# Performance work log

Measured on AMD Instinct MI355X. Metric: run time of the kernel, lower is better.

Reference implementation:

```python
import jax, jax.numpy as jnp
from jax import lax
import numpy as np

LOWEST_HZ = 1.0
HIGHEST_HZ = 40.0
FS = 256
ORDER = 5


def _butter_sos(order, cutoff, btype, fs):
    """Butterworth digital filter as second-order sections (scipy-equivalent math)."""
    Wn = cutoff / (0.5 * fs)
    fs2 = 2.0
    warped = 2.0 * fs2 * np.tan(np.pi * Wn / fs2)  # pre-warped analog cutoff
    m = np.arange(1, order + 1)
    p = np.exp(1j * np.pi * (2 * m + order - 1) / (2.0 * order))  # analog prototype poles
    if btype == 'lp':
        z = np.zeros(0, dtype=complex)
        p = p * warped
        k = warped ** order
    else:  # 'hp' : lp2hp transform
        k = 1.0 / np.real(np.prod(-p))
        p = warped / p
        z = np.zeros(order, dtype=complex)
    # bilinear transform (internal fs = 2)
    f2 = 2.0 * fs2
    pd = (f2 + p) / (f2 - p)
    zd = (f2 + z) / (f2 - z)
    kd = k * np.real(np.prod(f2 - z) / np.prod(f2 - p))
    zd = np.concatenate([zd, -np.ones(order - len(zd))])  # pad zeros at z=-1
    z0 = float(np.real(zd[0]))  # all digital zeros identical (z=-1 for lp, z=+1 for hp)
    real_p = [float(pp.real) for pp in pd if abs(pp.imag) < 1e-10]
    cplx_p = [pp for pp in pd if pp.imag > 1e-10]
    sos = []
    for pp in cplx_p:  # conjugate pair -> one biquad
        sos.append([1.0, -2.0 * z0, z0 * z0, 1.0, -2.0 * pp.real, float(np.real(pp * np.conj(pp)))])
    for pr in real_p:  # leftover real pole -> first-order section
        sos.append([1.0, -z0, 0.0, 1.0, -pr, 0.0])
    sos = np.array(sos, dtype=np.float64)
    sos[0, :3] *= kd  # fold overall gain into first section
    return sos


def _sosfilt(sos, x):
    """Cascaded biquad IIR (direct form II transposed), zero initial state. x: [..., T]."""
    S = sos.shape[0]
    b0, b1, b2 = sos[:, 0], sos[:, 1], sos[:, 2]
    a1, a2 = sos[:, 4], sos[:, 5]
    xT = jnp.moveaxis(x, -1, 0)  # [T, ...]
    state0 = jnp.zeros((S, 2) + xT.shape[1:], x.dtype)

    def step(state, xt):
        cur = xt
        new = []
        for i in range(S):  # fixed small cascade of 6 sections
            w1, w2 = state[i, 0], state[i, 1]
            y = b0[i] * cur + w1
            nw1 = b1[i] * cur - a1[i] * y + w2
            nw2 = b2[i] * cur - a2[i] * y
            new.append(jnp.stack([nw1, nw2]))
            cur = y
        return jnp.stack(new), cur

    _, yT = lax.scan(step, state0, xT)
    return jnp.moveaxis(yT, 0, -1)


def setup_inputs() -> dict:
    key = jax.random.key(0)
    x = jax.random.normal(key, (32, 64, 16384), dtype=jnp.float32)
    sos_hp = _butter_sos(ORDER, LOWEST_HZ, 'hp', FS)
    sos_lp = _butter_sos(ORDER, HIGHEST_HZ, 'lp', FS)
    sos = jnp.asarray(np.concatenate([sos_hp, sos_lp], axis=0), dtype=jnp.float32)  # [6,6]
    return {"x": x, "sos": sos}


def reference(x, sos):
    # highpass sections then lowpass sections = one 6-section cascade
    return _sosfilt(sos, x)
```

## Files before the change

### kernel.cpp

```cpp
#include <hip/hip_runtime.h>

#define T_LEN 16384
#define NSEC 6
#define NSTATE 12
#define NMAT (NSTATE * NSTATE)
#define NPOW 5
#define NTHR 256
#define NS_TOT 2048

__device__ float g_Mp[NPOW * NMAT];
__device__ float g_Phi[64 * NSTATE];

__device__ __forceinline__ float rfl(float v) {
    return __int_as_float(__builtin_amdgcn_readfirstlane(__float_as_int(v)));
}

__global__ void k_matpow(const float* __restrict__ sos) {
    __shared__ double A[NMAT];
    __shared__ double ph[2][NSTATE];
    int tid = threadIdx.x;

    if (tid < NSTATE) {
        double b0[NSEC], b1[NSEC], b2[NSEC], a1[NSEC], a2[NSEC];
#pragma unroll
        for (int i = 0; i < NSEC; ++i) {
            b0[i] = (double)sos[i * 6 + 0];
            b1[i] = (double)sos[i * 6 + 1];
            b2[i] = (double)sos[i * 6 + 2];
            a1[i] = (double)sos[i * 6 + 4];
            a2[i] = (double)sos[i * 6 + 5];
        }
        double w1[NSEC], w2[NSEC];
#pragma unroll
        for (int i = 0; i < NSEC; ++i) {
            w1[i] = (tid == 2 * i) ? 1.0 : 0.0;
            w2[i] = (tid == 2 * i + 1) ? 1.0 : 0.0;
        }
        double cur = 0.0;
#pragma unroll
        for (int i = 0; i < NSEC; ++i) {
            double yv = fma(b0[i], cur, w1[i]);
            double n1 = fma(b1[i], cur, fma(-a1[i], yv, w2[i]));
            double n2 = fma(b2[i], cur, -(a2[i] * yv));
            w1[i] = n1; w2[i] = n2; cur = yv;
        }
#pragma unroll
        for (int i = 0; i < NSEC; ++i) {
            A[(2 * i) * NSTATE + tid]     = w1[i];
            A[(2 * i + 1) * NSTATE + tid] = w2[i];
        }
        double c = 0.0;
        if ((tid & 1) == 0) {
            int i = tid >> 1;
            double p = 1.0;
            for (int j = i + 1; j < NSEC; ++j) p *= (double)sos[j * 6 + 0];
            c = p;
        }
        ph[0][tid] = c;
    }
    __syncthreads();

    for (int t = 0; t < 64; ++t) {
        if (tid < NSTATE) {
            g_Phi[t * NSTATE + tid] = (float)ph[t & 1][tid];
            double v = 0.0;
#pragma unroll
            for (int kk = 0; kk < NSTATE; ++kk)
                v = fma(ph[t & 1][kk], A[kk * NSTATE + tid], v);
            ph[(t + 1) & 1][tid] = v;
        }
        __syncthreads();
    }

    const int rr = tid / NSTATE, cc = tid % NSTATE;
    for (int it = 1; it <= 10; ++it) {
        double v = 0.0;
        if (tid < NMAT) {
#pragma unroll
            for (int kk = 0; kk < NSTATE; ++kk)
                v = fma(A[rr * NSTATE + kk], A[kk * NSTATE + cc], v);
        }
        __syncthreads();
        if (tid < NMAT) {
            A[rr * NSTATE + cc] = v;
            if (it >= 6) g_Mp[(it - 6) * NMAT + tid] = (float)v;
        }
        __syncthreads();
    }
}

#define TRI_MATVEC(MROW_BASE, IN, OUT, INIT_FROM)                               \
    {                                                                           \
        _Pragma("unroll")                                                       \
        for (int q = 0; q < NSTATE; ++q) {                                      \
            const int lim = 2 * (q >> 1) + 2;                                   \
            const float4* row = (const float4*)((MROW_BASE) + q * NSTATE);      \
            float acc = (INIT_FROM);                                            \
            float4 r0 = row[0];                                                 \
            acc = fmaf(r0.x, (IN)[0], acc);                                     \
            acc = fmaf(r0.y, (IN)[1], acc);                                     \
            if (lim > 2) { acc = fmaf(r0.z, (IN)[2], acc);                      \
                           acc = fmaf(r0.w, (IN)[3], acc); }                    \
            if (lim > 4) {                                                      \
                float4 r1 = row[1];                                             \
                acc = fmaf(r1.x, (IN)[4], acc);                                 \
                acc = fmaf(r1.y, (IN)[5], acc);                                 \
                if (lim > 6) { acc = fmaf(r1.z, (IN)[6], acc);                  \
                               acc = fmaf(r1.w, (IN)[7], acc); }                \
            }                                                                   \
            if (lim > 8) {                                                      \
                float4 r2 = row[2];                                             \
                acc = fmaf(r2.x, (IN)[8], acc);                                 \
                acc = fmaf(r2.y, (IN)[9], acc);                                 \
                if (lim > 10) { acc = fmaf(r2.z, (IN)[10], acc);                \
                                acc = fmaf(r2.w, (IN)[11], acc); }              \
            }                                                                   \
            (OUT)[q] = acc;                                                     \
        }                                                                       \
    }

__global__ void __launch_bounds__(NTHR, 4)
k_main(const float* __restrict__ x, const float* __restrict__ sos,
       float* __restrict__ y) {
    __shared__ float Mp[NPOW][NMAT];
    __shared__ float Ph[64 * NSTATE];
    __shared__ float cw[4][NSTATE];
    __shared__ float4 sm4[2048];

    const int k = threadIdx.x;
    const int lane = k & 63;
    const int w = k >> 6;
    const int sig = blockIdx.x;

    for (int i = k; i < NPOW * NMAT; i += NTHR)
        Mp[i / NMAT][i % NMAT] = g_Mp[i];
    for (int i = k; i < 64 * NSTATE; i += NTHR)
        Ph[i] = g_Phi[i];

    float b0[NSEC], b1[NSEC], b2[NSEC], a1[NSEC], a2[NSEC];
#pragma unroll
    for (int i = 0; i < NSEC; ++i) {
        b0[i] = rfl(sos[i * 6 + 0]);
        b1[i] = rfl(sos[i * 6 + 1]);
        b2[i] = rfl(sos[i * 6 + 2]);
        a1[i] = rfl(sos[i * 6 + 4]);
        a2[i] = rfl(sos[i * 6 + 5]);
    }

    const float4* xp4 = (const float4*)(x + (size_t)sig * T_LEN) + k * 16;
    float4 stash[16];
    float w1_[NSEC], w2_[NSEC];
#pragma unroll
    for (int i = 0; i < NSEC; ++i) { w1_[i] = 0.f; w2_[i] = 0.f; }

    auto fstep = [&](float cur) -> float {
#pragma unroll
        for (int i = 0; i < NSEC; ++i) {
            float yv = fmaf(b0[i], cur, w1_[i]);
            w1_[i] = fmaf(b1[i], cur, fmaf(-a1[i], yv, w2_[i]));
            w2_[i] = fmaf(b2[i], cur, -(a2[i] * yv));
            cur = yv;
        }
        return cur;
    };

#pragma unroll
    for (int m = 0; m < 16; ++m) {
        float4 v = xp4[m];
        v.x = fstep(v.x); v.y = fstep(v.y); v.z = fstep(v.z); v.w = fstep(v.w);
        stash[m] = v;
    }
    float c0[NSTATE];
#pragma unroll
    for (int i = 0; i < NSEC; ++i) { c0[2 * i] = w1_[i]; c0[2 * i + 1] = w2_[i]; }

    __syncthreads();

#pragma unroll
    for (int rnd = 0; rnd < NPOW; ++rnd) {
        const int d = 1 << rnd;
        float pr[NSTATE];
#pragma unroll
        for (int j = 0; j < NSTATE; ++j) pr[j] = __shfl_up(c0[j], d, 64);
        if (lane >= d) {
            float nc[NSTATE];
            TRI_MATVEC(Mp[rnd], pr, nc, c0[q]);
#pragma unroll
            for (int j = 0; j < NSTATE; ++j) c0[j] = nc[j];
        }
    }

    if (lane == 63) {
#pragma unroll
        for (int j = 0; j < NSTATE; ++j) cw[w][j] = c0[j];
    }
    __syncthreads();

    if (w > 0) {
        float v[NSTATE];
#pragma unroll
        for (int j = 0; j < NSTATE; ++j) v[j] = cw[w - 1][j];
#pragma unroll
        for (int i = 0; i < NPOW; ++i) {
            if (((lane + 1) >> i) & 1) {
                float nv[NSTATE];
                TRI_MATVEC(Mp[i], v, nv, 0.f);
#pragma unroll
                for (int j = 0; j < NSTATE; ++j) v[j] = nv[j];
            }
        }
        if (lane < 31) {
#pragma unroll
            for (int j = 0; j < NSTATE; ++j) c0[j] += v[j];
        }
    }

    float si[NSTATE];
#pragma unroll
    for (int j = 0; j < NSTATE; ++j) si[j] = __shfl_up(c0[j], 1, 64);
    if (lane == 0) {
#pragma unroll
        for (int j = 0; j < NSTATE; ++j) si[j] = (w == 0) ? 0.f : cw[w - 1][j];
    }

#pragma unroll
    for (int m = 0; m < 16; ++m) {
        float4 v = stash[m];
        float corr[4];
#pragma unroll
        for (int q = 0; q < 4; ++q) {
            const float4* ph = (const float4*)&Ph[(m * 4 + q) * NSTATE];
            float4 p0 = ph[0], p1 = ph[1], p2 = ph[2];
            float acc = p0.x * si[0];
            acc = fmaf(p0.y, si[1], acc);
            acc = fmaf(p0.z, si[2], acc);
            acc = fmaf(p0.w, si[3], acc);
            acc = fmaf(p1.x, si[4], acc);
            acc = fmaf(p1.y, si[5], acc);
            acc = fmaf(p1.z, si[6], acc);
            acc = fmaf(p1.w, si[7], acc);
            acc = fmaf(p2.x, si[8], acc);
            acc = fmaf(p2.y, si[9], acc);
            acc = fmaf(p2.z, si[10], acc);
            acc = fmaf(p2.w, si[11], acc);
            corr[q] = acc;
        }
        v.x += corr[0]; v.y += corr[1]; v.z += corr[2]; v.w += corr[3];
        stash[m] = v;
    }

    float4* yp4 = (float4*)(y + (size_t)sig * T_LEN);
#pragma unroll 1
    for (int r = 0; r < 2; ++r) {
        __syncthreads();
        if ((w >> 1) == r) {
            const int base = (w & 1) * 1024;
#pragma unroll
            for (int m = 0; m < 16; ++m)
                sm4[base + lane * 16 + (m ^ (lane & 15))] = stash[m];
        }
        __syncthreads();
#pragma unroll
        for (int q = 0; q < 8; ++q) {
            int j = k + 256 * q;
            int s = (j & ~15) | ((j ^ (j >> 4)) & 15);
            yp4[r * 2048 + j] = sm4[s];
        }
    }
}

extern "C" void kernel_launch(void* const* d_in, const int* in_sizes, int n_in,
                              void* d_out, int out_size, void* d_ws, size_t ws_size,
                              hipStream_t stream) {
    const float* x   = (const float*)d_in[0];
    const float* sos = (const float*)d_in[1];
    if (n_in >= 2 && in_sizes[0] <= 256 && in_sizes[1] > 256) {
        x = (const float*)d_in[1];
        sos = (const float*)d_in[0];
    }
    float* out = (float*)d_out;

    int NS = out_size / T_LEN;
    if (NS > NS_TOT) NS = NS_TOT;
    if (NS < 1) NS = 1;

    k_matpow<<<1, 256, 0, stream>>>(sos);
    k_main<<<NS, NTHR, 0, stream>>>(x, sos, out);
}
```

Measured before the change: 98.06 us.

## Halve per-thread chunk to 32 samples and double block threads to 512

Each block now uses 512 threads, each filtering 32 samples instead of 64. This halves the serial recurrence length per thread, reduces the stash register footprint, and raises occupancy via launch bounds of 8. The prefix scan gains a sixth power level, and the cross-wave carry now folds the previous wave's state into the shifted start state using lane bits. The matvec is done in place, and the smem transpose swizzle is adapted to 8 float4 per thread. The tradeoff is more scan work and more matvec rounds per element.

```diff
diff --git a/kernel.cpp b/kernel.cpp
--- a/kernel.cpp
+++ b/kernel.cpp
@@ -4,12 +4,13 @@
 #define NSEC 6
 #define NSTATE 12
 #define NMAT (NSTATE * NSTATE)
-#define NPOW 5
-#define NTHR 256
+#define L_SMP 32
+#define NPOW 6
+#define NTHR 512
 #define NS_TOT 2048
 
 __device__ float g_Mp[NPOW * NMAT];
-__device__ float g_Phi[64 * NSTATE];
+__device__ float g_Phi[L_SMP * NSTATE];
 
 __device__ __forceinline__ float rfl(float v) {
     return __int_as_float(__builtin_amdgcn_readfirstlane(__float_as_int(v)));
@@ -60,7 +61,7 @@
     }
     __syncthreads();
 
-    for (int t = 0; t < 64; ++t) {
+    for (int t = 0; t < L_SMP; ++t) {
         if (tid < NSTATE) {
             g_Phi[t * NSTATE + tid] = (float)ph[t & 1][tid];
             double v = 0.0;
@@ -83,48 +84,53 @@
         __syncthreads();
         if (tid < NMAT) {
             A[rr * NSTATE + cc] = v;
-            if (it >= 6) g_Mp[(it - 6) * NMAT + tid] = (float)v;
-        }
-        __syncthreads();
-    }
-}
-
-#define TRI_MATVEC(MROW_BASE, IN, OUT, INIT_FROM)                               \
+            if (it >= 5) g_Mp[(it - 5) * NMAT + tid] = (float)v;
+        }
+        __syncthreads();
+    }
+}
+
+#define TRI_MATVEC_IP(MBASE, V, EXTRA0, EXTRA1)                                 \
     {                                                                           \
         _Pragma("unroll")                                                       \
-        for (int q = 0; q < NSTATE; ++q) {                                      \
-            const int lim = 2 * (q >> 1) + 2;                                   \
-            const float4* row = (const float4*)((MROW_BASE) + q * NSTATE);      \
-            float acc = (INIT_FROM);                                            \
-            float4 r0 = row[0];                                                 \
-            acc = fmaf(r0.x, (IN)[0], acc);                                     \
-            acc = fmaf(r0.y, (IN)[1], acc);                                     \
-            if (lim > 2) { acc = fmaf(r0.z, (IN)[2], acc);                      \
-                           acc = fmaf(r0.w, (IN)[3], acc); }                    \
-            if (lim > 4) {                                                      \
-                float4 r1 = row[1];                                             \
-                acc = fmaf(r1.x, (IN)[4], acc);                                 \
-                acc = fmaf(r1.y, (IN)[5], acc);                                 \
-                if (lim > 6) { acc = fmaf(r1.z, (IN)[6], acc);                  \
-                               acc = fmaf(r1.w, (IN)[7], acc); }                \
+        for (int p = 5; p >= 0; --p) {                                          \
+            float o0, o1;                                                       \
+            _Pragma("unroll")                                                   \
+            for (int rq = 0; rq < 2; ++rq) {                                    \
+                const int q = 2 * p + rq;                                       \
+                const float4* row = (const float4*)((MBASE) + q * NSTATE);      \
+                float acc = (rq == 0 ? (EXTRA0) : (EXTRA1));                    \
+                float4 r0 = row[0];                                             \
+                acc = fmaf(r0.x, (V)[0], acc);                                  \
+                acc = fmaf(r0.y, (V)[1], acc);                                  \
+                if (p >= 1) { acc = fmaf(r0.z, (V)[2], acc);                    \
+                              acc = fmaf(r0.w, (V)[3], acc); }                  \
+                if (p >= 2) {                                                   \
+                    float4 r1 = row[1];                                         \
+                    acc = fmaf(r1.x, (V)[4], acc);                              \
+                    acc = fmaf(r1.y, (V)[5], acc);                              \
+                    if (p >= 3) { acc = fmaf(r1.z, (V)[6], acc);                \
+                                  acc = fmaf(r1.w, (V)[7], acc); }              \
+                }                                                               \
+                if (p >= 4) {                                                   \
+                    float4 r2 = row[2];                                         \
+                    acc = fmaf(r2.x, (V)[8], acc);                              \
+                    acc = fmaf(r2.y, (V)[9], acc);                              \
+                    if (p >= 5) { acc = fmaf(r2.z, (V)[10], acc);               \
+                                  acc = fmaf(r2.w, (V)[11], acc); }             \
+                }                                                               \
+                if (rq == 0) o0 = acc; else o1 = acc;                           \
             }                                                                   \
-            if (lim > 8) {                                                      \
-                float4 r2 = row[2];                                             \
-                acc = fmaf(r2.x, (IN)[8], acc);                                 \
-                acc = fmaf(r2.y, (IN)[9], acc);                                 \
-                if (lim > 10) { acc = fmaf(r2.z, (IN)[10], acc);                \
-                                acc = fmaf(r2.w, (IN)[11], acc); }              \
-            }                                                                   \
-            (OUT)[q] = acc;                                                     \
+            (V)[2 * p] = o0; (V)[2 * p + 1] = o1;                               \
         }                                                                       \
     }
 
-__global__ void __launch_bounds__(NTHR, 4)
+__global__ void __launch_bounds__(NTHR, 8)
 k_main(const float* __restrict__ x, const float* __restrict__ sos,
        float* __restrict__ y) {
     __shared__ float Mp[NPOW][NMAT];
-    __shared__ float Ph[64 * NSTATE];
-    __shared__ float cw[4][NSTATE];
+    __shared__ float Ph[L_SMP * NSTATE];
+    __shared__ float cw[8][NSTATE];
     __shared__ float4 sm4[2048];
 
     const int k = threadIdx.x;
@@ -134,7 +140,7 @@
 
     for (int i = k; i < NPOW * NMAT; i += NTHR)
         Mp[i / NMAT][i % NMAT] = g_Mp[i];
-    for (int i = k; i < 64 * NSTATE; i += NTHR)
+    for (int i = k; i < L_SMP * NSTATE; i += NTHR)
         Ph[i] = g_Phi[i];
 
     float b0[NSEC], b1[NSEC], b2[NSEC], a1[NSEC], a2[NSEC];
@@ -147,8 +153,8 @@
         a2[i] = rfl(sos[i * 6 + 5]);
     }
 
-    const float4* xp4 = (const float4*)(x + (size_t)sig * T_LEN) + k * 16;
-    float4 stash[16];
+    const float4* xp4 = (const float4*)(x + (size_t)sig * T_LEN) + k * (L_SMP / 4);
+    float4 stash[L_SMP / 4];
     float w1_[NSEC], w2_[NSEC];
 #pragma unroll
     for (int i = 0; i < NSEC; ++i) { w1_[i] = 0.f; w2_[i] = 0.f; }
@@ -165,7 +171,7 @@
     };
 
 #pragma unroll
-    for (int m = 0; m < 16; ++m) {
+    for (int m = 0; m < L_SMP / 4; ++m) {
         float4 v = xp4[m];
         v.x = fstep(v.x); v.y = fstep(v.y); v.z = fstep(v.z); v.w = fstep(v.w);
         stash[m] = v;
@@ -183,10 +189,9 @@
 #pragma unroll
         for (int j = 0; j < NSTATE; ++j) pr[j] = __shfl_up(c0[j], d, 64);
         if (lane >= d) {
-            float nc[NSTATE];
-            TRI_MATVEC(Mp[rnd], pr, nc, c0[q]);
-#pragma unroll
-            for (int j = 0; j < NSTATE; ++j) c0[j] = nc[j];
+            TRI_MATVEC_IP(Mp[rnd], pr, c0[2 * p], c0[2 * p + 1]);
+#pragma unroll
+            for (int j = 0; j < NSTATE; ++j) c0[j] = pr[j];
         }
     }
 
@@ -196,35 +201,28 @@
     }
     __syncthreads();
 
+    float si[NSTATE];
+#pragma unroll
+    for (int j = 0; j < NSTATE; ++j) {
+        si[j] = __shfl_up(c0[j], 1, 64);
+        if (lane == 0) si[j] = 0.f;
+    }
     if (w > 0) {
-        float v[NSTATE];
-#pragma unroll
-        for (int j = 0; j < NSTATE; ++j) v[j] = cw[w - 1][j];
+        float u[NSTATE];
+#pragma unroll
+        for (int j = 0; j < NSTATE; ++j) u[j] = cw[w - 1][j];
 #pragma unroll
         for (int i = 0; i < NPOW; ++i) {
-            if (((lane + 1) >> i) & 1) {
-                float nv[NSTATE];
-                TRI_MATVEC(Mp[i], v, nv, 0.f);
-#pragma unroll
-                for (int j = 0; j < NSTATE; ++j) v[j] = nv[j];
+            if ((lane >> i) & 1) {
+                TRI_MATVEC_IP(Mp[i], u, 0.f, 0.f);
             }
         }
-        if (lane < 31) {
-#pragma unroll
-            for (int j = 0; j < NSTATE; ++j) c0[j] += v[j];
-        }
-    }
-
-    float si[NSTATE];
-#pragma unroll
-    for (int j = 0; j < NSTATE; ++j) si[j] = __shfl_up(c0[j], 1, 64);
-    if (lane == 0) {
-#pragma unroll
-        for (int j = 0; j < NSTATE; ++j) si[j] = (w == 0) ? 0.f : cw[w - 1][j];
-    }
-
-#pragma unroll
-    for (int m = 0; m < 16; ++m) {
+#pragma unroll
+        for (int j = 0; j < NSTATE; ++j) si[j] += u[j];
+    }
+
+#pragma unroll
+    for (int m = 0; m < L_SMP / 4; ++m) {
         float4 v = stash[m];
         float corr[4];
 #pragma unroll
@@ -253,17 +251,17 @@
 #pragma unroll 1
     for (int r = 0; r < 2; ++r) {
         __syncthreads();
-        if ((w >> 1) == r) {
-            const int base = (w & 1) * 1024;
-#pragma unroll
-            for (int m = 0; m < 16; ++m)
-                sm4[base + lane * 16 + (m ^ (lane & 15))] = stash[m];
-        }
-        __syncthreads();
-#pragma unroll
-        for (int q = 0; q < 8; ++q) {
-            int j = k + 256 * q;
-            int s = (j & ~15) | ((j ^ (j >> 4)) & 15);
+        if ((k >> 8) == r) {
+            const int t8 = k & 255;
+#pragma unroll
+            for (int m = 0; m < L_SMP / 4; ++m)
+                sm4[t8 * 8 + (m ^ (t8 & 7))] = stash[m];
+        }
+        __syncthreads();
+#pragma unroll
+        for (int q = 0; q < 4; ++q) {
+            int j = k + NTHR * q;
+            int s = (j & ~7) | ((j ^ (j >> 3)) & 7);
             yp4[r * 2048 + j] = sm4[s];
         }
     }
```

Measured after the change: 141.1 us. 43.9% more time.
